# Optimization experiments

Hardware: AMD Instinct MI355X
Metric: run time of the kernel (lower is better)

## Reference

```python
import jax, jax.numpy as jnp
import numpy as np

MAX_WEIGHT = 10.0  # config.max_weight
EPS = 1e-8

BATCH = 2048
VOCAB = 256
SEQ_LEN = 64
NUM_DENDRITES = SEQ_LEN * VOCAB  # 16384


def setup_inputs() -> dict:
    key = jax.random.key(0)
    k1, k2 = jax.random.split(key)
    # binary dendrite activations in {0,1}, stored as float32 as in the torch module
    binary = jax.random.randint(k1, (BATCH, NUM_DENDRITES), 0, 2).astype(jnp.float32)
    # raw_weights ~ Uniform(-1, 1) per nn.init.uniform_
    raw_weights = jax.random.uniform(k2, (VOCAB, NUM_DENDRITES), dtype=jnp.float32,
                                     minval=-1.0, maxval=1.0)
    return {"binary": binary, "raw_weights": raw_weights}


def reference(binary, raw_weights):
    # bounded positive weights: max_weight * sigmoid(raw)
    w = MAX_WEIGHT * jax.nn.sigmoid(raw_weights)            # (vocab, D)
    log_w = jnp.log(jnp.clip(w, EPS))                       # (vocab, D)
    # masked log-sum: where binary==0 the torch code uses log(1)=0, then multiplies
    # by binary anyway, so it is exactly binary @ log_w.T
    log_sum = jnp.einsum('bd,vd->bv', binary, log_w)        # (batch, vocab)
    n_active = jnp.clip(jnp.sum(binary, axis=-1, keepdims=True), 1.0)  # (batch, 1)
    logits = jnp.exp(log_sum / n_active)                    # geometric mean of fired weights
    return logits
```

## Files before the change

### kernel.cpp

```cpp
#include <hip/hip_runtime.h>

#define BATCH 2048
#define VOCAB 256
#define KDIM 16384
#define BM 32
#define BK 32
#define KCHUNK 1024
#define NT (KCHUNK / BK)
#define NKCH (KDIM / KCHUNK)
#define LN10 2.302585092994046f

typedef __attribute__((ext_vector_type(8))) short short8;
typedef __attribute__((ext_vector_type(4))) float f32x4;

__device__ __forceinline__ unsigned short f2bf_rne(float f) {
  unsigned int u = __float_as_uint(f);
  u += 0x7fffu + ((u >> 16) & 1u);
  return (unsigned short)(u >> 16);
}
__device__ __forceinline__ unsigned int pack2(float lo, float hi) {
  return (__float_as_uint(lo) >> 16) | (__float_as_uint(hi) & 0xffff0000u);
}

__device__ __forceinline__ void async16(void* lds, const void* g) {
  __builtin_amdgcn_global_load_lds(
      (const __attribute__((address_space(1))) unsigned int*)g,
      (__attribute__((address_space(3))) unsigned int*)lds, 16, 0, 0);
}

__global__ __launch_bounds__(256) void k_logw(const float* __restrict__ raw,
                                              unsigned short* __restrict__ logw) {
  int i = blockIdx.x * 256 + threadIdx.x;
  float4 x = ((const float4*)raw)[i];
  ushort4 r;
  r.x = f2bf_rne(LN10 - log1pf(expf(-x.x)));
  r.y = f2bf_rne(LN10 - log1pf(expf(-x.y)));
  r.z = f2bf_rne(LN10 - log1pf(expf(-x.z)));
  r.w = f2bf_rne(LN10 - log1pf(expf(-x.w)));
  ((ushort4*)logw)[i] = r;
}

__global__ __launch_bounds__(256, 4) void k_gemm(
    const float* __restrict__ binary, const unsigned short* __restrict__ logw,
    float* __restrict__ accb, float* __restrict__ nact) {
  __shared__ char smem[36864];
  char* const Ab0 = smem;
  char* const Ab1 = smem + 2048;
  char* const Bb0 = smem + 4096;
  char* const Bb1 = smem + 20480;

  const int tid = threadIdx.x;
  const int wv = tid >> 6;
  const int lane = tid & 63;
  const int l15 = lane & 15;
  const int lhi = lane >> 4;
  const int m0 = blockIdx.x * BM;
  const int k0 = blockIdx.y * KCHUNK;

  const int ar = tid >> 3, ac = tid & 7;
  const float* a_src = binary + (size_t)(m0 + ar) * KDIM + k0 + ac * 4;
  const int aw = ar * 64 + ((((ac >> 1) ^ (ar & 3)) << 4) | ((ac & 1) << 3));

  const int br = lane >> 2;
  const int bs = (lane & 3) ^ (br & 3);
  const unsigned short* b_src =
      logw + (size_t)(wv * 64 + br) * KDIM + k0 + bs * 8;

  float4 areg;
  float asum = 0.f;
  f32x4 acc[2][4];
#pragma unroll
  for (int m = 0; m < 2; ++m)
#pragma unroll
    for (int n = 0; n < 4; ++n) acc[m][n] = f32x4{0.f, 0.f, 0.f, 0.f};

  auto A_LOAD = [&](int t) { areg = *(const float4*)(a_src + t * BK); };
  auto A_WRITE = [&](char* A) {
    asum += areg.x + areg.y + areg.z + areg.w;
    uint2 u;
    u.x = pack2(areg.x, areg.y);
    u.y = pack2(areg.z, areg.w);
    *(uint2*)(A + aw) = u;
  };
  auto B_STAGE = [&](int t, char* B) {
#pragma unroll
    for (int i = 0; i < 4; ++i)
      async16(B + wv * 4096 + i * 1024, b_src + (size_t)i * 16 * KDIM + t * BK);
  };
  auto COMPUTE = [&](const char* A, const char* B) {
    const int sw = (lhi ^ (l15 & 3)) << 4;
    short8 af[2], bfr[4];
    af[0] = *(const short8*)(A + l15 * 64 + sw);
    af[1] = *(const short8*)(A + (16 + l15) * 64 + sw);
#pragma unroll
    for (int n = 0; n < 4; ++n)
      bfr[n] = *(const short8*)(B + (wv * 64 + n * 16 + l15) * 64 + sw);
#pragma unroll
    for (int m = 0; m < 2; ++m)
#pragma unroll
      for (int n = 0; n < 4; ++n)
        acc[m][n] = __builtin_amdgcn_mfma_f32_16x16x32_bf16(af[m], bfr[n],
                                                            acc[m][n], 0, 0, 0);
  };

  A_LOAD(0);
  B_STAGE(0, Bb0);
  A_WRITE(Ab0);
  __syncthreads();

#pragma unroll 1
  for (int t = 0; t < NT; t += 2) {
    A_LOAD(t + 1);
    B_STAGE(t + 1, Bb1);
    COMPUTE(Ab0, Bb0);
    A_WRITE(Ab1);
    __syncthreads();
    if (t + 2 < NT) {
      A_LOAD(t + 2);
      B_STAGE(t + 2, Bb0);
    }
    COMPUTE(Ab1, Bb1);
    if (t + 2 < NT) A_WRITE(Ab0);
    __syncthreads();
  }

  float s = asum;
  s += __shfl_xor(s, 1, 64);
  s += __shfl_xor(s, 2, 64);
  s += __shfl_xor(s, 4, 64);
  if ((lane & 7) == 0) atomicAdd(&nact[m0 + (tid >> 3)], s);

#pragma unroll
  for (int m = 0; m < 2; ++m)
#pragma unroll
    for (int n = 0; n < 4; ++n)
#pragma unroll
      for (int i = 0; i < 4; ++i) {
        int r = m0 + m * 16 + lhi * 4 + i;
        int c = wv * 64 + n * 16 + l15;
        atomicAdd(&accb[(size_t)r * VOCAB + c], acc[m][n][i]);
      }
}

__global__ __launch_bounds__(256) void k_out(float* __restrict__ io,
                                             const float* __restrict__ nact) {
  int b = blockIdx.x;
  int v = threadIdx.x;
  float n = fmaxf(nact[b], 1.0f);
  size_t idx = (size_t)b * VOCAB + v;
  io[idx] = expf(io[idx] / n);
}

extern "C" void kernel_launch(void* const* d_in, const int* in_sizes, int n_in,
                              void* d_out, int out_size, void* d_ws, size_t ws_size,
                              hipStream_t stream) {
  const float* binary = (const float*)d_in[0];
  const float* raw = (const float*)d_in[1];
  float* out = (float*)d_out;
  char* ws = (char*)d_ws;
  unsigned short* logw = (unsigned short*)ws;
  float* nact = (float*)(ws + (size_t)8 * 1024 * 1024);

  hipMemsetAsync(out, 0, (size_t)BATCH * VOCAB * sizeof(float), stream);
  hipMemsetAsync(nact, 0, BATCH * sizeof(float), stream);

  k_logw<<<(VOCAB * KDIM / 4) / 256, 256, 0, stream>>>(raw, logw);

  dim3 g(BATCH / BM, NKCH);
  k_gemm<<<g, 256, 0, stream>>>(binary, logw, out, nact);

  k_out<<<BATCH, VOCAB, 0, stream>>>(out, nact);
}
```

Baseline: 272.4 us.

## Enlarge GEMM block tile, load A fragments directly to registers, manual async pipeline

Raises the block M tile from 32 to 128 rows and halves the K chunk, so each wave owns 32 batch rows across the full vocab (32 accumulators) instead of a 64-column slice. The binary A operand now goes straight from global memory into MFMA operand registers, with no LDS staging. B is double-buffered through async global-to-LDS loads, synchronised with explicit vmcnt waits and raw s_barrier. This cuts LDS traffic for A and reloads of B per batch row, at the cost of much higher register pressure (128 accumulator floats), lower occupancy, and more atomics per block.

```diff
diff --git a/kernel.cpp b/kernel.cpp
--- a/kernel.cpp
+++ b/kernel.cpp
@@ -3,15 +3,17 @@
 #define BATCH 2048
 #define VOCAB 256
 #define KDIM 16384
-#define BM 32
+#define BM 128
 #define BK 32
-#define KCHUNK 1024
+#define KCHUNK 512
 #define NT (KCHUNK / BK)
 #define NKCH (KDIM / KCHUNK)
 #define LN10 2.302585092994046f
 
 typedef __attribute__((ext_vector_type(8))) short short8;
 typedef __attribute__((ext_vector_type(4))) float f32x4;
+
+#define FENCE asm volatile("" ::: "memory")
 
 __device__ __forceinline__ unsigned short f2bf_rne(float f) {
   unsigned int u = __float_as_uint(f);
@@ -40,14 +42,11 @@
   ((ushort4*)logw)[i] = r;
 }
 
-__global__ __launch_bounds__(256, 4) void k_gemm(
+__global__ __launch_bounds__(256) void k_gemm(
     const float* __restrict__ binary, const unsigned short* __restrict__ logw,
     float* __restrict__ accb, float* __restrict__ nact) {
-  __shared__ char smem[36864];
-  char* const Ab0 = smem;
-  char* const Ab1 = smem + 2048;
-  char* const Bb0 = smem + 4096;
-  char* const Bb1 = smem + 20480;
+  __shared__ char Bsm0[16384];
+  __shared__ char Bsm1[16384];
 
   const int tid = threadIdx.x;
   const int wv = tid >> 6;
@@ -57,87 +56,101 @@
   const int m0 = blockIdx.x * BM;
   const int k0 = blockIdx.y * KCHUNK;
 
-  const int ar = tid >> 3, ac = tid & 7;
-  const float* a_src = binary + (size_t)(m0 + ar) * KDIM + k0 + ac * 4;
-  const int aw = ar * 64 + ((((ac >> 1) ^ (ar & 3)) << 4) | ((ac & 1) << 3));
+  const int brow = lane >> 2;
+  const int bks = (lane & 3) ^ ((lane >> 3) & 3);
+  const unsigned short* bsrc =
+      logw + (size_t)(wv * 64 + brow) * KDIM + k0 + bks * 8;
 
-  const int br = lane >> 2;
-  const int bs = (lane & 3) ^ (br & 3);
-  const unsigned short* b_src =
-      logw + (size_t)(wv * 64 + br) * KDIM + k0 + bs * 8;
+  const float* asrc0 = binary + (size_t)(m0 + wv * 32 + l15) * KDIM + k0 + lhi * 8;
+  const float* asrc1 = asrc0 + (size_t)16 * KDIM;
 
-  float4 areg;
-  float asum = 0.f;
-  f32x4 acc[2][4];
+  const int rdoff = l15 * 64 + ((lhi ^ ((l15 >> 1) & 3)) << 4);
+
+  f32x4 acc[2][16];
 #pragma unroll
   for (int m = 0; m < 2; ++m)
 #pragma unroll
-    for (int n = 0; n < 4; ++n) acc[m][n] = f32x4{0.f, 0.f, 0.f, 0.f};
+    for (int n = 0; n < 16; ++n) acc[m][n] = f32x4{0.f, 0.f, 0.f, 0.f};
+  float s0 = 0.f, s1 = 0.f;
+  float4 Ae[4], Ao[4];
 
-  auto A_LOAD = [&](int t) { areg = *(const float4*)(a_src + t * BK); };
-  auto A_WRITE = [&](char* A) {
-    asum += areg.x + areg.y + areg.z + areg.w;
-    uint2 u;
-    u.x = pack2(areg.x, areg.y);
-    u.y = pack2(areg.z, areg.w);
-    *(uint2*)(A + aw) = u;
-  };
   auto B_STAGE = [&](int t, char* B) {
 #pragma unroll
     for (int i = 0; i < 4; ++i)
-      async16(B + wv * 4096 + i * 1024, b_src + (size_t)i * 16 * KDIM + t * BK);
+      async16(B + (wv * 4 + i) * 1024, bsrc + (size_t)i * 16 * KDIM + t * BK);
   };
-  auto COMPUTE = [&](const char* A, const char* B) {
-    const int sw = (lhi ^ (l15 & 3)) << 4;
-    short8 af[2], bfr[4];
-    af[0] = *(const short8*)(A + l15 * 64 + sw);
-    af[1] = *(const short8*)(A + (16 + l15) * 64 + sw);
+  auto A_LOAD = [&](int t, float4* A) {
+    const float4* p0 = (const float4*)(asrc0 + t * BK);
+    const float4* p1 = (const float4*)(asrc1 + t * BK);
+    A[0] = p0[0]; A[1] = p0[1]; A[2] = p1[0]; A[3] = p1[1];
+  };
+  auto COMPUTE = [&](const float4* A, const char* B) {
+    s0 += A[0].x + A[0].y + A[0].z + A[0].w + A[1].x + A[1].y + A[1].z + A[1].w;
+    s1 += A[2].x + A[2].y + A[2].z + A[2].w + A[3].x + A[3].y + A[3].z + A[3].w;
+    union { short8 s; unsigned int u[4]; } a0, a1;
+    a0.u[0] = pack2(A[0].x, A[0].y); a0.u[1] = pack2(A[0].z, A[0].w);
+    a0.u[2] = pack2(A[1].x, A[1].y); a0.u[3] = pack2(A[1].z, A[1].w);
+    a1.u[0] = pack2(A[2].x, A[2].y); a1.u[1] = pack2(A[2].z, A[2].w);
+    a1.u[2] = pack2(A[3].x, A[3].y); a1.u[3] = pack2(A[3].z, A[3].w);
 #pragma unroll
-    for (int n = 0; n < 4; ++n)
-      bfr[n] = *(const short8*)(B + (wv * 64 + n * 16 + l15) * 64 + sw);
-#pragma unroll
-    for (int m = 0; m < 2; ++m)
-#pragma unroll
-      for (int n = 0; n < 4; ++n)
-        acc[m][n] = __builtin_amdgcn_mfma_f32_16x16x32_bf16(af[m], bfr[n],
-                                                            acc[m][n], 0, 0, 0);
+    for (int n = 0; n < 16; ++n) {
+      short8 b = *(const short8*)(B + n * 1024 + rdoff);
+      acc[0][n] = __builtin_amdgcn_mfma_f32_16x16x32_bf16(a0.s, b, acc[0][n], 0, 0, 0);
+      acc[1][n] = __builtin_amdgcn_mfma_f32_16x16x32_bf16(a1.s, b, acc[1][n], 0, 0, 0);
+    }
   };
 
-  A_LOAD(0);
-  B_STAGE(0, Bb0);
-  A_WRITE(Ab0);
-  __syncthreads();
+  B_STAGE(0, Bsm0);
+  FENCE;
+  A_LOAD(0, Ae);
+  FENCE;
 
 #pragma unroll 1
   for (int t = 0; t < NT; t += 2) {
-    A_LOAD(t + 1);
-    B_STAGE(t + 1, Bb1);
-    COMPUTE(Ab0, Bb0);
-    A_WRITE(Ab1);
-    __syncthreads();
+    FENCE;
+    __builtin_amdgcn_s_barrier();
+    FENCE;
+    B_STAGE(t + 1, Bsm1);
+    FENCE;
+    A_LOAD(t + 1, Ao);
+    FENCE;
+    asm volatile("s_waitcnt vmcnt(8)" ::: "memory");
+    __builtin_amdgcn_s_barrier();
+    FENCE;
+    COMPUTE(Ae, Bsm0);
+    FENCE;
+    __builtin_amdgcn_s_barrier();
+    FENCE;
     if (t + 2 < NT) {
-      A_LOAD(t + 2);
-      B_STAGE(t + 2, Bb0);
+      B_STAGE(t + 2, Bsm0);
+      FENCE;
+      A_LOAD(t + 2, Ae);
+      FENCE;
+      asm volatile("s_waitcnt vmcnt(8)" ::: "memory");
+    } else {
+      asm volatile("s_waitcnt vmcnt(0)" ::: "memory");
     }
-    COMPUTE(Ab1, Bb1);
-    if (t + 2 < NT) A_WRITE(Ab0);
-    __syncthreads();
+    __builtin_amdgcn_s_barrier();
+    FENCE;
+    COMPUTE(Ao, Bsm1);
   }
 
-  float s = asum;
-  s += __shfl_xor(s, 1, 64);
-  s += __shfl_xor(s, 2, 64);
-  s += __shfl_xor(s, 4, 64);
-  if ((lane & 7) == 0) atomicAdd(&nact[m0 + (tid >> 3)], s);
+  float t0 = s0, t1 = s1;
+  t0 += __shfl_xor(t0, 16, 64); t0 += __shfl_xor(t0, 32, 64);
+  t1 += __shfl_xor(t1, 16, 64); t1 += __shfl_xor(t1, 32, 64);
+  if (lane < 16) {
+    atomicAdd(&nact[m0 + wv * 32 + l15], t0);
+    atomicAdd(&nact[m0 + wv * 32 + 16 + l15], t1);
+  }
 
 #pragma unroll
   for (int m = 0; m < 2; ++m)
 #pragma unroll
-    for (int n = 0; n < 4; ++n)
+    for (int n = 0; n < 16; ++n)
 #pragma unroll
       for (int i = 0; i < 4; ++i) {
-        int r = m0 + m * 16 + lhi * 4 + i;
-        int c = wv * 64 + n * 16 + l15;
+        int r = m0 + wv * 32 + m * 16 + lhi * 4 + i;
+        int c = n * 16 + l15;
         atomicAdd(&accb[(size_t)r * VOCAB + c], acc[m][n][i]);
       }
 }
```

Measured after the change: 272.5 us. No clear change (+0.0%).
